# Performance work log

Hardware: AMD Instinct MI355X
Metric: run time of the kernel (lower is better)

## Reference

```python
import jax, jax.numpy as jnp
import numpy as np
import math

D_MODEL = 1024
N_HEADS = 16
D_K = D_MODEL // N_HEADS
BS, SQ, SK = 2, 2048, 2048


def setup_inputs() -> dict:
    key = jax.random.key(0)
    ks = jax.random.split(key, 7)
    q = jax.random.normal(ks[0], (BS, SQ, D_MODEL), dtype=jnp.float32)
    k = jax.random.normal(ks[1], (BS, SK, D_MODEL), dtype=jnp.float32)
    v = jax.random.normal(ks[2], (BS, SK, D_MODEL), dtype=jnp.float32)
    # causal mask: True = masked out (matches torch masked_fill semantics)
    mask = jnp.broadcast_to(
        ~jnp.tril(jnp.ones((SQ, SK), dtype=bool)), (BS, SQ, SK))
    scale = 1.0 / math.sqrt(D_MODEL)
    wq = jax.random.normal(ks[3], (D_MODEL, D_MODEL), dtype=jnp.float32) * scale
    wk = jax.random.normal(ks[4], (D_MODEL, D_MODEL), dtype=jnp.float32) * scale
    wv = jax.random.normal(ks[5], (D_MODEL, D_MODEL), dtype=jnp.float32) * scale
    wo = jax.random.normal(ks[6], (D_MODEL, D_MODEL), dtype=jnp.float32) * scale
    return {"q": q, "k": k, "v": v, "mask": mask,
            "wq": wq, "wk": wk, "wv": wv, "wo": wo}


def reference(q, k, v, mask, wq, wk, wv, wo):
    bs, sq, _ = q.shape
    sk = k.shape[1]
    # nn.Linear(bias=False): x @ W.T ; reshape to heads -> [b, h, s, d_k]
    qh = (q @ wq.T).reshape(bs, sq, N_HEADS, D_K).transpose(0, 2, 1, 3)
    kh = (k @ wk.T).reshape(bs, sk, N_HEADS, D_K).transpose(0, 2, 1, 3)
    vh = (v @ wv.T).reshape(bs, sk, N_HEADS, D_K).transpose(0, 2, 1, 3)
    # scaled dot-product attention, full [b,h,sq,sk] scores (as original)
    z = jnp.einsum('bhqd,bhkd->bhqk', qh, kh) / math.sqrt(D_K)
    z = jnp.where(mask[:, None, :, :], jnp.float32(-1e10), z)
    z = jax.nn.softmax(z, axis=-1)
    z = jnp.einsum('bhqk,bhkd->bhqd', z, vh)
    z = z.transpose(0, 2, 1, 3).reshape(bs, sq, D_MODEL)
    return z @ wo.T
```

## Files before the change

kernel.cpp:

```cpp
#include <hip/hip_runtime.h>
#include <hip/hip_bf16.h>
#include <stdint.h>

typedef short s16x8 __attribute__((ext_vector_type(8)));
typedef float f32x4 __attribute__((ext_vector_type(4)));

#define BSZ 2
#define SQL 2048
#define DMODEL 1024
#define NHEAD 16
#define DKH 64

#if __has_builtin(__builtin_amdgcn_exp2f)
#define EXP2(x) __builtin_amdgcn_exp2f(x)
#else
#define EXP2(x) exp2f(x)
#endif

__device__ __forceinline__ ushort f2bf(float f) {
  uint32_t u = __float_as_uint(f);
  u += 0x7fffu + ((u >> 16) & 1u);
  return (ushort)(u >> 16);
}

__device__ __forceinline__ uint32_t cvtpk_bf16(float lo, float hi) {
  uint32_t r;
  asm("v_cvt_pk_bf16_f32 %0, %1, %2" : "=v"(r) : "v"(lo), "v"(hi));
  return r;
}

__device__ __forceinline__ float rowmax16(float x) {
  x = fmaxf(x, __int_as_float(__builtin_amdgcn_update_dpp(0, __float_as_int(x), 0x121, 0xf, 0xf, true)));
  x = fmaxf(x, __int_as_float(__builtin_amdgcn_update_dpp(0, __float_as_int(x), 0x122, 0xf, 0xf, true)));
  x = fmaxf(x, __int_as_float(__builtin_amdgcn_update_dpp(0, __float_as_int(x), 0x124, 0xf, 0xf, true)));
  x = fmaxf(x, __int_as_float(__builtin_amdgcn_update_dpp(0, __float_as_int(x), 0x128, 0xf, 0xf, true)));
  return x;
}

__device__ __forceinline__ void gload_lds16(const ushort* g, ushort* l) {
  __builtin_amdgcn_global_load_lds((const __attribute__((address_space(1))) void*)g,
                                   (__attribute__((address_space(3))) void*)l,
                                   16, 0, 0);
}

__global__ void cvt_all(const float* __restrict__ q, const float* __restrict__ k,
                        const float* __restrict__ v, const float* __restrict__ wq,
                        const float* __restrict__ wk, const float* __restrict__ wv,
                        const float* __restrict__ wo, ushort* __restrict__ dq,
                        ushort* __restrict__ dk, ushort* __restrict__ dv,
                        ushort* __restrict__ dwq, ushort* __restrict__ dwk,
                        ushort* __restrict__ dwv, ushort* __restrict__ dwo) {
  int b = blockIdx.x;
  const float* s; ushort* d; int off;
  if (b < 4096)       { s = q;  d = dq;  off = b; }
  else if (b < 8192)  { s = k;  d = dk;  off = b - 4096; }
  else if (b < 12288) { s = v;  d = dv;  off = b - 8192; }
  else if (b < 13312) { s = wq; d = dwq; off = b - 12288; }
  else if (b < 14336) { s = wk; d = dwk; off = b - 13312; }
  else if (b < 15360) { s = wv; d = dwv; off = b - 14336; }
  else                { s = wo; d = dwo; off = b - 15360; }
  int i = (off * 256 + threadIdx.x) * 4;
  float4 x = *(const float4*)(s + i);
  ushort4 o;
  o.x = f2bf(x.x); o.y = f2bf(x.y); o.z = f2bf(x.z); o.w = f2bf(x.w);
  *(ushort4*)(d + i) = o;
}

__device__ __forceinline__ void gemm_core(const ushort* __restrict__ A,
                                          const ushort* __restrict__ B,
                                          ushort* sA, ushort* sB, f32x4 (&acc)[4][4]) {
  const int t = threadIdx.x, w = t >> 6, lane = t & 63;
  const int lrow = lane & 15, g = lane >> 4;
  const int swz = (lrow >> 1) & 3;
  const int m0 = blockIdx.x * 128, n0 = blockIdx.y * 128;
  const int wm = (w >> 1) * 64, wn = (w & 1) * 64;

  auto stage = [&](int kt, int buf) {
#pragma unroll
    for (int i = 0; i < 2; ++i) {
      int ci = i * 256 + t;
      int row = ci >> 2;
      int cs = (ci & 3) ^ ((row >> 1) & 3);
      gload_lds16(A + (size_t)(m0 + row) * 1024 + kt * 32 + cs * 8,
                  sA + buf * 4096 + (i * 256 + w * 64) * 8);
      gload_lds16(B + (size_t)(n0 + row) * 1024 + kt * 32 + cs * 8,
                  sB + buf * 4096 + (i * 256 + w * 64) * 8);
    }
  };

  stage(0, 0);
  for (int kt = 0; kt < 32; ++kt) {
    const int cur = kt & 1;
    if (kt < 31) {
      stage(kt + 1, cur ^ 1);
      asm volatile("s_waitcnt vmcnt(4)" ::: "memory");
    } else {
      asm volatile("s_waitcnt vmcnt(0)" ::: "memory");
    }
    __builtin_amdgcn_s_barrier();
    __builtin_amdgcn_sched_barrier(0);
    const ushort* pA = sA + cur * 4096;
    const ushort* pB = sB + cur * 4096;
    const int gs = (g ^ swz) * 8;
    s16x8 af[4], bfr[4];
#pragma unroll
    for (int mi = 0; mi < 4; ++mi)
      af[mi] = *(const s16x8*)(pA + (wm + mi * 16 + lrow) * 32 + gs);
#pragma unroll
    for (int ni = 0; ni < 4; ++ni)
      bfr[ni] = *(const s16x8*)(pB + (wn + ni * 16 + lrow) * 32 + gs);
    __builtin_amdgcn_s_setprio(1);
#pragma unroll
    for (int mi = 0; mi < 4; ++mi)
#pragma unroll
      for (int ni = 0; ni < 4; ++ni)
        acc[mi][ni] = __builtin_amdgcn_mfma_f32_16x16x32_bf16(af[mi], bfr[ni], acc[mi][ni], 0, 0, 0);
    __builtin_amdgcn_s_setprio(0);
    asm volatile("s_waitcnt lgkmcnt(0)" ::: "memory");
    __builtin_amdgcn_s_barrier();
  }
}

__device__ __forceinline__ void epi_heads(f32x4 (&acc)[4][4], ushort* D, float scale, bool vtrans) {
  const int lane = threadIdx.x & 63, w = threadIdx.x >> 6;
  const int m0 = blockIdx.x * 128, n0 = blockIdx.y * 128;
  const int wm = (w >> 1) * 64, wn = (w & 1) * 64;
#pragma unroll
  for (int mi = 0; mi < 4; ++mi)
#pragma unroll
    for (int ni = 0; ni < 4; ++ni)
#pragma unroll
      for (int r = 0; r < 4; ++r) {
        int m = m0 + wm + mi * 16 + (lane >> 4) * 4 + r;
        int n = n0 + wn + ni * 16 + (lane & 15);
        ushort bv = f2bf(acc[mi][ni][r] * scale);
        int b = m >> 11, s = m & 2047, h = n >> 6, d = n & 63;
        if (vtrans) {
          int sp = (s & ~63) | (((s & 15) << 2) | ((s >> 4) & 3));
          D[((size_t)((b * 16 + h) * 64 + d)) * 2048 + sp] = bv;
        } else {
          D[((size_t)((b * 16 + h) * 2048 + s)) * 64 + d] = bv;
        }
      }
}

__global__ __launch_bounds__(256) void gemm_qkv(const ushort* __restrict__ qb,
                                                const ushort* __restrict__ kb,
                                                const ushort* __restrict__ vb,
                                                const ushort* __restrict__ wqb,
                                                const ushort* __restrict__ wkb,
                                                const ushort* __restrict__ wvb,
                                                ushort* __restrict__ Qh,
                                                ushort* __restrict__ Kh,
                                                ushort* __restrict__ Vt) {
  __shared__ __align__(16) ushort sA[2 * 4096];
  __shared__ __align__(16) ushort sB[2 * 4096];
  const int z = blockIdx.z;
  const ushort* A = (z == 0) ? qb : (z == 1) ? kb : vb;
  const ushort* B = (z == 0) ? wqb : (z == 1) ? wkb : wvb;
  f32x4 acc[4][4] = {};
  gemm_core(A, B, sA, sB, acc);
  ushort* D = (z == 0) ? Qh : (z == 1) ? Kh : Vt;
  epi_heads(acc, D, (z == 0) ? 0.18033688f : 1.0f, z == 2);
}

__global__ __launch_bounds__(256) void gemm_out64(const ushort* __restrict__ A,
                                                  const ushort* __restrict__ B,
                                                  float* __restrict__ D) {
  __shared__ __align__(16) ushort sA[2 * 2048];
  __shared__ __align__(16) ushort sB[2 * 4096];
  const int t = threadIdx.x, w = t >> 6, lane = t & 63;
  const int lrow = lane & 15, g = lane >> 4;
  const int swz = (lrow >> 1) & 3;
  const int m0 = blockIdx.x * 64, n0 = blockIdx.y * 128;
  const int wm = (w >> 1) * 32, wn = (w & 1) * 64;
  f32x4 acc[2][4] = {};

  auto stage = [&](int kt, int buf) {
    {
      int row = t >> 2;
      int cs = (t & 3) ^ ((row >> 1) & 3);
      gload_lds16(A + (size_t)(m0 + row) * 1024 + kt * 32 + cs * 8,
                  sA + buf * 2048 + (w * 64) * 8);
    }
#pragma unroll
    for (int i = 0; i < 2; ++i) {
      int ci = i * 256 + t;
      int row = ci >> 2;
      int cs = (ci & 3) ^ ((row >> 1) & 3);
      gload_lds16(B + (size_t)(n0 + row) * 1024 + kt * 32 + cs * 8,
                  sB + buf * 4096 + (i * 256 + w * 64) * 8);
    }
  };

  stage(0, 0);
  for (int kt = 0; kt < 32; ++kt) {
    const int cur = kt & 1;
    if (kt < 31) {
      stage(kt + 1, cur ^ 1);
      asm volatile("s_waitcnt vmcnt(3)" ::: "memory");
    } else {
      asm volatile("s_waitcnt vmcnt(0)" ::: "memory");
    }
    __builtin_amdgcn_s_barrier();
    __builtin_amdgcn_sched_barrier(0);
    const ushort* pA = sA + cur * 2048;
    const ushort* pB = sB + cur * 4096;
    const int gs = (g ^ swz) * 8;
    s16x8 af[2], bfr[4];
#pragma unroll
    for (int mi = 0; mi < 2; ++mi)
      af[mi] = *(const s16x8*)(pA + (wm + mi * 16 + lrow) * 32 + gs);
#pragma unroll
    for (int ni = 0; ni < 4; ++ni)
      bfr[ni] = *(const s16x8*)(pB + (wn + ni * 16 + lrow) * 32 + gs);
    __builtin_amdgcn_s_setprio(1);
#pragma unroll
    for (int mi = 0; mi < 2; ++mi)
#pragma unroll
      for (int ni = 0; ni < 4; ++ni)
        acc[mi][ni] = __builtin_amdgcn_mfma_f32_16x16x32_bf16(af[mi], bfr[ni], acc[mi][ni], 0, 0, 0);
    __builtin_amdgcn_s_setprio(0);
    asm volatile("s_waitcnt lgkmcnt(0)" ::: "memory");
    __builtin_amdgcn_s_barrier();
  }

#pragma unroll
  for (int mi = 0; mi < 2; ++mi)
#pragma unroll
    for (int ni = 0; ni < 4; ++ni)
#pragma unroll
      for (int r = 0; r < 4; ++r) {
        int m = m0 + wm + mi * 16 + (lane >> 4) * 4 + r;
        int n = n0 + wn + ni * 16 + (lane & 15);
        D[(size_t)m * 1024 + n] = acc[mi][ni][r];
      }
}

__global__ __launch_bounds__(512) void attn_fwd(const ushort* __restrict__ Qh,
                                                const ushort* __restrict__ Kh,
                                                const ushort* __restrict__ Vt,
                                                ushort* __restrict__ Z) {
  __shared__ __align__(16) ushort sK[2][64 * 64];
  __shared__ __align__(16) ushort sV[2][64 * 64];
  __shared__ __align__(16) ushort sP[8][16 * 72];
  const int t = threadIdx.x, w = t >> 6, lane = t & 63;
  const int lcol = lane & 15, lhi = lane >> 4;
  const int p = blockIdx.x, bh = blockIdx.y;
  const int qlo = p, qhi = 31 - p;
  const int setid = w >> 2;
  const int qtile = setid ? qhi : qlo;
  const int qr0 = qtile * 64 + (w & 3) * 16;
  const ushort* Qb = Qh + (size_t)bh * SQL * DKH;
  const ushort* Kb = Kh + (size_t)bh * SQL * DKH;
  const ushort* Vb = Vt + (size_t)bh * DKH * SQL;

  s16x8 qf0, qf1;
  {
    const ushort* qp = Qb + (size_t)(qr0 + lcol) * DKH + lhi * 8;
    qf0 = *(const s16x8*)qp;
    qf1 = *(const s16x8*)(qp + 32);
  }
  float mr[4], lrp[4];
  f32x4 o[4] = {};
#pragma unroll
  for (int r = 0; r < 4; ++r) { mr[r] = -1e30f; lrp[r] = 0.f; }
  ushort* Pw = &sP[w][0];

  auto stage = [&](int kb, int buf) {
    int row = t >> 3, cc = t & 7;
    int scz = cc ^ (row & 7);
    gload_lds16(Kb + (size_t)(kb * 64 + row) * DKH + scz * 8, &sK[buf][w * 512]);
    gload_lds16(Vb + (size_t)row * SQL + kb * 64 + scz * 8, &sV[buf][w * 512]);
  };

  const int nkb = qhi + 1;
  stage(0, 0);
  for (int kb = 0; kb < nkb; ++kb) {
    const int cur = kb & 1;
    if (kb + 1 < nkb) {
      stage(kb + 1, cur ^ 1);
      asm volatile("s_waitcnt vmcnt(2)" ::: "memory");
    } else {
      asm volatile("s_waitcnt vmcnt(0)" ::: "memory");
    }
    __builtin_amdgcn_s_barrier();
    __builtin_amdgcn_sched_barrier(0);
    const bool act = setid || (kb <= qlo);
    if (act) {
      const ushort* pK = &sK[cur][0];
      const ushort* pV = &sV[cur][0];
      f32x4 sc4[4];
      __builtin_amdgcn_s_setprio(1);
#pragma unroll
      for (int ktt = 0; ktt < 4; ++ktt) {
        int row = ktt * 16 + lcol;
        int c0 = lhi ^ (row & 7);
        int c1 = (lhi + 4) ^ (row & 7);
        s16x8 k0 = *(const s16x8*)(pK + row * 64 + c0 * 8);
        s16x8 k1 = *(const s16x8*)(pK + row * 64 + c1 * 8);
        f32x4 a = {};
        a = __builtin_amdgcn_mfma_f32_16x16x32_bf16(qf0, k0, a, 0, 0, 0);
        a = __builtin_amdgcn_mfma_f32_16x16x32_bf16(qf1, k1, a, 0, 0, 0);
        sc4[ktt] = a;
      }
      __builtin_amdgcn_s_setprio(0);
      if (kb == qtile) {
#pragma unroll
        for (int ktt = 0; ktt < 4; ++ktt) {
          int kloc = ktt * 16 + lcol;
#pragma unroll
          for (int r = 0; r < 4; ++r)
            if (kloc > (w & 3) * 16 + lhi * 4 + r) sc4[ktt][r] = -1e30f;
        }
      }
      float tm4[4];
#pragma unroll
      for (int r = 0; r < 4; ++r) {
        float tm = fmaxf(fmaxf(sc4[0][r], sc4[1][r]), fmaxf(sc4[2][r], sc4[3][r]));
        tm4[r] = rowmax16(tm);
      }
      bool grow = (tm4[0] > mr[0] + 8.f) || (tm4[1] > mr[1] + 8.f) ||
                  (tm4[2] > mr[2] + 8.f) || (tm4[3] > mr[3] + 8.f);
      if (__any((int)grow)) {
#pragma unroll
        for (int r = 0; r < 4; ++r) {
          float mn = fmaxf(mr[r], tm4[r]);
          float al = EXP2(mr[r] - mn);
          lrp[r] *= al;
          o[0][r] *= al; o[1][r] *= al; o[2][r] *= al; o[3][r] *= al;
          mr[r] = mn;
        }
      }
#pragma unroll
      for (int r = 0; r < 4; ++r) {
        float p0 = EXP2(sc4[0][r] - mr[r]);
        float p1 = EXP2(sc4[1][r] - mr[r]);
        float p2 = EXP2(sc4[2][r] - mr[r]);
        float p3 = EXP2(sc4[3][r] - mr[r]);
        lrp[r] += (p0 + p1) + (p2 + p3);
        uint2 pk;
        pk.x = cvtpk_bf16(p0, p1);
        pk.y = cvtpk_bf16(p2, p3);
        *(uint2*)(Pw + (lhi * 4 + r) * 72 + lcol * 4) = pk;
      }
      __builtin_amdgcn_s_setprio(1);
#pragma unroll
      for (int kc = 0; kc < 2; ++kc) {
        s16x8 pf = *(const s16x8*)(Pw + lcol * 72 + kc * 32 + lhi * 8);
#pragma unroll
        for (int dt = 0; dt < 4; ++dt) {
          int row = dt * 16 + lcol;
          int cc = (lhi + 4 * kc) ^ (row & 7);
          s16x8 vf = *(const s16x8*)(pV + row * 64 + cc * 8);
          o[dt] = __builtin_amdgcn_mfma_f32_16x16x32_bf16(pf, vf, o[dt], 0, 0, 0);
        }
      }
      __builtin_amdgcn_s_setprio(0);
    }
    asm volatile("s_waitcnt lgkmcnt(0)" ::: "memory");
    __builtin_amdgcn_s_barrier();
  }

  const int b = bh >> 4, h = bh & 15;
#pragma unroll
  for (int r = 0; r < 4; ++r) {
    float sum = lrp[r];
    sum += __shfl_xor(sum, 1);
    sum += __shfl_xor(sum, 2);
    sum += __shfl_xor(sum, 4);
    sum += __shfl_xor(sum, 8);
    float inv = 1.0f / sum;
    int q = qr0 + lhi * 4 + r;
    size_t base = ((size_t)(b * SQL + q)) * DMODEL + h * DKH + lcol;
#pragma unroll
    for (int dt = 0; dt < 4; ++dt)
      Z[base + dt * 16] = f2bf(o[dt][r] * inv);
  }
}

extern "C" void kernel_launch(void* const* d_in, const int* in_sizes, int n_in,
                              void* d_out, int out_size, void* d_ws, size_t ws_size,
                              hipStream_t stream) {
  const float* q = (const float*)d_in[0];
  const float* k = (const float*)d_in[1];
  const float* v = (const float*)d_in[2];
  const float* wq = (const float*)d_in[4];
  const float* wk = (const float*)d_in[5];
  const float* wv = (const float*)d_in[6];
  const float* wo = (const float*)d_in[7];

  const size_t NBIG = (size_t)BSZ * SQL * DMODEL;
  const size_t NW = (size_t)DMODEL * DMODEL;
  ushort* qb = (ushort*)d_ws;
  ushort* kb = qb + NBIG;
  ushort* vb = kb + NBIG;
  ushort* wqb = vb + NBIG;
  ushort* wkb = wqb + NW;
  ushort* wvb = wkb + NW;
  ushort* wob = wvb + NW;
  ushort* Qh = wob + NW;
  ushort* Kh = Qh + NBIG;
  ushort* Vt = Kh + NBIG;
  ushort* Z  = Vt + NBIG;

  cvt_all<<<dim3(16384), 256, 0, stream>>>(q, k, v, wq, wk, wv, wo,
                                           qb, kb, vb, wqb, wkb, wvb, wob);
  gemm_qkv<<<dim3(32, 8, 3), 256, 0, stream>>>(qb, kb, vb, wqb, wkb, wvb, Qh, Kh, Vt);
  attn_fwd<<<dim3(16, BSZ * NHEAD), 512, 0, stream>>>(Qh, Kh, Vt, Z);
  gemm_out64<<<dim3(64, 8), 256, 0, stream>>>(Z, wob, (float*)d_out);
}
```

Before: 129.8 us.

## Fuse fp32-to-bf16 activation conversion into QKV GEMM and remap attention block order

Removes the separate conversion pass over q/k/v. The QKV GEMM now stages fp32 activations directly into LDS with an XOR swizzle and converts them to bf16 while building the MFMA fragments, and only the weights are still pre-converted. This avoids writing and rereading the bf16 copies of the large activations, at the cost of double the LDS footprint and load traffic for the A tile plus conversion ALU work in the inner loop. The attention kernel also remaps its block indices so that consecutive blocks land on different heads, changing scheduling and cache locality.

```diff
diff --git a/kernel.cpp b/kernel.cpp
--- a/kernel.cpp
+++ b/kernel.cpp
@@ -43,82 +43,17 @@
                                    16, 0, 0);
 }
 
-__global__ void cvt_all(const float* __restrict__ q, const float* __restrict__ k,
-                        const float* __restrict__ v, const float* __restrict__ wq,
-                        const float* __restrict__ wk, const float* __restrict__ wv,
-                        const float* __restrict__ wo, ushort* __restrict__ dq,
-                        ushort* __restrict__ dk, ushort* __restrict__ dv,
-                        ushort* __restrict__ dwq, ushort* __restrict__ dwk,
-                        ushort* __restrict__ dwv, ushort* __restrict__ dwo) {
-  int b = blockIdx.x;
-  const float* s; ushort* d; int off;
-  if (b < 4096)       { s = q;  d = dq;  off = b; }
-  else if (b < 8192)  { s = k;  d = dk;  off = b - 4096; }
-  else if (b < 12288) { s = v;  d = dv;  off = b - 8192; }
-  else if (b < 13312) { s = wq; d = dwq; off = b - 12288; }
-  else if (b < 14336) { s = wk; d = dwk; off = b - 13312; }
-  else if (b < 15360) { s = wv; d = dwv; off = b - 14336; }
-  else                { s = wo; d = dwo; off = b - 15360; }
-  int i = (off * 256 + threadIdx.x) * 4;
+__global__ void cvt_w(const float* __restrict__ wq, const float* __restrict__ wk,
+                      const float* __restrict__ wv, const float* __restrict__ wo,
+                      ushort* __restrict__ dwq, ushort* __restrict__ dwk,
+                      ushort* __restrict__ dwv, ushort* __restrict__ dwo) {
+  const float* s = (blockIdx.y == 0) ? wq : (blockIdx.y == 1) ? wk : (blockIdx.y == 2) ? wv : wo;
+  ushort* d = (blockIdx.y == 0) ? dwq : (blockIdx.y == 1) ? dwk : (blockIdx.y == 2) ? dwv : dwo;
+  int i = (blockIdx.x * 256 + threadIdx.x) * 4;
   float4 x = *(const float4*)(s + i);
   ushort4 o;
   o.x = f2bf(x.x); o.y = f2bf(x.y); o.z = f2bf(x.z); o.w = f2bf(x.w);
   *(ushort4*)(d + i) = o;
-}
-
-__device__ __forceinline__ void gemm_core(const ushort* __restrict__ A,
-                                          const ushort* __restrict__ B,
-                                          ushort* sA, ushort* sB, f32x4 (&acc)[4][4]) {
-  const int t = threadIdx.x, w = t >> 6, lane = t & 63;
-  const int lrow = lane & 15, g = lane >> 4;
-  const int swz = (lrow >> 1) & 3;
-  const int m0 = blockIdx.x * 128, n0 = blockIdx.y * 128;
-  const int wm = (w >> 1) * 64, wn = (w & 1) * 64;
-
-  auto stage = [&](int kt, int buf) {
-#pragma unroll
-    for (int i = 0; i < 2; ++i) {
-      int ci = i * 256 + t;
-      int row = ci >> 2;
-      int cs = (ci & 3) ^ ((row >> 1) & 3);
-      gload_lds16(A + (size_t)(m0 + row) * 1024 + kt * 32 + cs * 8,
-                  sA + buf * 4096 + (i * 256 + w * 64) * 8);
-      gload_lds16(B + (size_t)(n0 + row) * 1024 + kt * 32 + cs * 8,
-                  sB + buf * 4096 + (i * 256 + w * 64) * 8);
-    }
-  };
-
-  stage(0, 0);
-  for (int kt = 0; kt < 32; ++kt) {
-    const int cur = kt & 1;
-    if (kt < 31) {
-      stage(kt + 1, cur ^ 1);
-      asm volatile("s_waitcnt vmcnt(4)" ::: "memory");
-    } else {
-      asm volatile("s_waitcnt vmcnt(0)" ::: "memory");
-    }
-    __builtin_amdgcn_s_barrier();
-    __builtin_amdgcn_sched_barrier(0);
-    const ushort* pA = sA + cur * 4096;
-    const ushort* pB = sB + cur * 4096;
-    const int gs = (g ^ swz) * 8;
-    s16x8 af[4], bfr[4];
-#pragma unroll
-    for (int mi = 0; mi < 4; ++mi)
-      af[mi] = *(const s16x8*)(pA + (wm + mi * 16 + lrow) * 32 + gs);
-#pragma unroll
-    for (int ni = 0; ni < 4; ++ni)
-      bfr[ni] = *(const s16x8*)(pB + (wn + ni * 16 + lrow) * 32 + gs);
-    __builtin_amdgcn_s_setprio(1);
-#pragma unroll
-    for (int mi = 0; mi < 4; ++mi)
-#pragma unroll
-      for (int ni = 0; ni < 4; ++ni)
-        acc[mi][ni] = __builtin_amdgcn_mfma_f32_16x16x32_bf16(af[mi], bfr[ni], acc[mi][ni], 0, 0, 0);
-    __builtin_amdgcn_s_setprio(0);
-    asm volatile("s_waitcnt lgkmcnt(0)" ::: "memory");
-    __builtin_amdgcn_s_barrier();
-  }
 }
 
 __device__ __forceinline__ void epi_heads(f32x4 (&acc)[4][4], ushort* D, float scale, bool vtrans) {
@@ -144,22 +79,89 @@
       }
 }
 
-__global__ __launch_bounds__(256) void gemm_qkv(const ushort* __restrict__ qb,
-                                                const ushort* __restrict__ kb,
-                                                const ushort* __restrict__ vb,
+__global__ __launch_bounds__(256) void gemm_qkv(const float* __restrict__ qf,
+                                                const float* __restrict__ kf,
+                                                const float* __restrict__ vf,
                                                 const ushort* __restrict__ wqb,
                                                 const ushort* __restrict__ wkb,
                                                 const ushort* __restrict__ wvb,
                                                 ushort* __restrict__ Qh,
                                                 ushort* __restrict__ Kh,
                                                 ushort* __restrict__ Vt) {
-  __shared__ __align__(16) ushort sA[2 * 4096];
+  __shared__ __align__(16) float sA32[2 * 4096];
   __shared__ __align__(16) ushort sB[2 * 4096];
   const int z = blockIdx.z;
-  const ushort* A = (z == 0) ? qb : (z == 1) ? kb : vb;
+  const float* A = (z == 0) ? qf : (z == 1) ? kf : vf;
   const ushort* B = (z == 0) ? wqb : (z == 1) ? wkb : wvb;
+  const int t = threadIdx.x, w = t >> 6, lane = t & 63;
+  const int lrow = lane & 15, g = lane >> 4;
+  const int swzB = (lrow >> 1) & 3;
+  const int m0 = blockIdx.x * 128, n0 = blockIdx.y * 128;
+  const int wm = (w >> 1) * 64, wn = (w & 1) * 64;
   f32x4 acc[4][4] = {};
-  gemm_core(A, B, sA, sB, acc);
+
+  auto stage = [&](int kt, int buf) {
+#pragma unroll
+    for (int i2 = 0; i2 < 4; ++i2) {
+      int ci = i2 * 256 + t;
+      int row = ci >> 3;
+      int fc = (ci & 7) ^ (row & 7);
+      gload_lds16((const ushort*)(A + (size_t)(m0 + row) * 1024 + kt * 32 + fc * 4),
+                  (ushort*)(sA32 + buf * 4096 + (i2 * 256 + w * 64) * 4));
+    }
+#pragma unroll
+    for (int i2 = 0; i2 < 2; ++i2) {
+      int ci = i2 * 256 + t;
+      int row = ci >> 2;
+      int cs = (ci & 3) ^ ((row >> 1) & 3);
+      gload_lds16(B + (size_t)(n0 + row) * 1024 + kt * 32 + cs * 8,
+                  sB + buf * 4096 + (i2 * 256 + w * 64) * 8);
+    }
+  };
+
+  stage(0, 0);
+  for (int kt = 0; kt < 32; ++kt) {
+    const int cur = kt & 1;
+    if (kt < 31) {
+      stage(kt + 1, cur ^ 1);
+      asm volatile("s_waitcnt vmcnt(6)" ::: "memory");
+    } else {
+      asm volatile("s_waitcnt vmcnt(0)" ::: "memory");
+    }
+    __builtin_amdgcn_s_barrier();
+    __builtin_amdgcn_sched_barrier(0);
+    const float* pA = sA32 + cur * 4096;
+    const ushort* pB = sB + cur * 4096;
+    const int gs = (g ^ swzB) * 8;
+    s16x8 af[4], bfr[4];
+#pragma unroll
+    for (int mi = 0; mi < 4; ++mi) {
+      int row = wm + mi * 16 + lrow;
+      int f0 = (2 * g) ^ (row & 7);
+      int f1 = (2 * g + 1) ^ (row & 7);
+      f32x4 x0 = *(const f32x4*)(pA + row * 32 + f0 * 4);
+      f32x4 x1 = *(const f32x4*)(pA + row * 32 + f1 * 4);
+      union { uint32_t u[4]; s16x8 v; } cc;
+      cc.u[0] = cvtpk_bf16(x0[0], x0[1]);
+      cc.u[1] = cvtpk_bf16(x0[2], x0[3]);
+      cc.u[2] = cvtpk_bf16(x1[0], x1[1]);
+      cc.u[3] = cvtpk_bf16(x1[2], x1[3]);
+      af[mi] = cc.v;
+    }
+#pragma unroll
+    for (int ni = 0; ni < 4; ++ni)
+      bfr[ni] = *(const s16x8*)(pB + (wn + ni * 16 + lrow) * 32 + gs);
+    __builtin_amdgcn_s_setprio(1);
+#pragma unroll
+    for (int mi = 0; mi < 4; ++mi)
+#pragma unroll
+      for (int ni = 0; ni < 4; ++ni)
+        acc[mi][ni] = __builtin_amdgcn_mfma_f32_16x16x32_bf16(af[mi], bfr[ni], acc[mi][ni], 0, 0, 0);
+    __builtin_amdgcn_s_setprio(0);
+    asm volatile("s_waitcnt lgkmcnt(0)" ::: "memory");
+    __builtin_amdgcn_s_barrier();
+  }
+
   ushort* D = (z == 0) ? Qh : (z == 1) ? Kh : Vt;
   epi_heads(acc, D, (z == 0) ? 0.18033688f : 1.0f, z == 2);
 }
@@ -184,12 +186,12 @@
                   sA + buf * 2048 + (w * 64) * 8);
     }
 #pragma unroll
-    for (int i = 0; i < 2; ++i) {
-      int ci = i * 256 + t;
+    for (int i2 = 0; i2 < 2; ++i2) {
+      int ci = i2 * 256 + t;
       int row = ci >> 2;
       int cs = (ci & 3) ^ ((row >> 1) & 3);
       gload_lds16(B + (size_t)(n0 + row) * 1024 + kt * 32 + cs * 8,
-                  sB + buf * 4096 + (i * 256 + w * 64) * 8);
+                  sB + buf * 4096 + (i2 * 256 + w * 64) * 8);
     }
   };
 
@@ -246,7 +248,9 @@
   __shared__ __align__(16) ushort sP[8][16 * 72];
   const int t = threadIdx.x, w = t >> 6, lane = t & 63;
   const int lcol = lane & 15, lhi = lane >> 4;
-  const int p = blockIdx.x, bh = blockIdx.y;
+  const int lid = blockIdx.x + 16 * blockIdx.y;
+  const int p = lid >> 5;
+  const int bh = (lid & 7) * 4 + ((lid >> 3) & 3);
   const int qlo = p, qhi = 31 - p;
   const int setid = w >> 2;
   const int qtile = setid ? qhi : qlo;
@@ -392,10 +396,7 @@
 
   const size_t NBIG = (size_t)BSZ * SQL * DMODEL;
   const size_t NW = (size_t)DMODEL * DMODEL;
-  ushort* qb = (ushort*)d_ws;
-  ushort* kb = qb + NBIG;
-  ushort* vb = kb + NBIG;
-  ushort* wqb = vb + NBIG;
+  ushort* wqb = (ushort*)d_ws;
   ushort* wkb = wqb + NW;
   ushort* wvb = wkb + NW;
   ushort* wob = wvb + NW;
@@ -404,9 +405,8 @@
   ushort* Vt = Kh + NBIG;
   ushort* Z  = Vt + NBIG;
 
-  cvt_all<<<dim3(16384), 256, 0, stream>>>(q, k, v, wq, wk, wv, wo,
-                                           qb, kb, vb, wqb, wkb, wvb, wob);
-  gemm_qkv<<<dim3(32, 8, 3), 256, 0, stream>>>(qb, kb, vb, wqb, wkb, wvb, Qh, Kh, Vt);
+  cvt_w<<<dim3(1024, 4), 256, 0, stream>>>(wq, wk, wv, wo, wqb, wkb, wvb, wob);
+  gemm_qkv<<<dim3(32, 8, 3), 256, 0, stream>>>(q, k, v, wqb, wkb, wvb, Qh, Kh, Vt);
   attn_fwd<<<dim3(16, BSZ * NHEAD), 512, 0, stream>>>(Qh, Kh, Vt, Z);
   gemm_out64<<<dim3(64, 8), 256, 0, stream>>>(Z, wob, (float*)d_out);
 }
```

Result: faster. 120.8 us, median of 3 (-6.9%).
